# Kernel optimization log

Measured on AMD Instinct MI355X. Metric: run time of the kernel, lower is better.

The kernel has to match this reference:

```python
import jax, jax.numpy as jnp
import numpy as np

N_ITER = 4
NEG = -1e9


def _build_distmask(n):
    # dists='' -> 2 groups: upper triangular (j>i) and lower triangular (j<i); diag excluded
    iu = jnp.triu(jnp.ones((n, n), jnp.float32), 1)
    return jnp.stack([iu, iu.T], axis=0)  # (2, n, n)


def setup_inputs() -> dict:
    key = jax.random.key(0)
    k1, k2, k3 = jax.random.split(key, 3)
    B, N, D, H, G = 16, 256, 128, 8, 64
    x = jax.random.normal(k1, (B, N, D), jnp.float32)
    mask = jnp.ones((B, N), jnp.int32)
    ternary = jax.random.normal(k2, (2, D, D, H), jnp.float32)
    global_ = jax.random.normal(k3, (G, D, H), jnp.float32) / np.sqrt(D).astype(np.float32)
    return {"x": x, "mask": mask, "ternary": ternary, "global_": global_}


def reference(x, mask, ternary, global_):
    # x: (B,N,D) unary scores; mask: (B,N); ternary: (2,D,D,H); global_: (G,D,H)
    B, N, D = x.shape
    dm = _build_distmask(N)                       # (2,N,N)
    m1 = mask != 0                                # (B,N) valid tokens
    m2 = m1[:, :, None] & m1[:, None, :]          # (B,N,N) valid pairs
    pair_bias = jnp.where(m2[:, None, :, :], 0.0, NEG)  # (B,1,N,N); global cols stay unmasked

    Q_Z = x
    for _ in range(N_ITER):
        qz = jax.nn.softmax(Q_Z, axis=-1)         # (B,N,D) q(Z_i)
        # left[k,b,i,c,h] = sum_a qz[b,i,a] * ternary[k,a,c,h]
        left = jnp.einsum('bia,kach->kbich', qz, ternary)
        # H-node scores over local candidates: F[b,h,i,j] = sum_k dm[k,i,j] * sum_c left[k,b,i,c,h] qz[b,j,c]
        Fk = jnp.einsum('kbich,bjc->kbhij', left, qz)
        F = jnp.einsum('kbhij,kij->bhij', Fk, dm) + pair_bias
        # H-node scores over global candidates: G[b,h,i,g] = sum_a qz[b,i,a] global_[g,a,h]
        Gs = jnp.einsum('bia,gah->bhig', qz, global_)
        S = jnp.concatenate([F, Gs], axis=-1)     # (B,H,N,N+G), all-attn: joint softmax
        qh = jax.nn.softmax(S, axis=-1)           # async update: fresh q(H) used for Z update
        qh_loc, qh_glb = qh[..., :N], qh[..., N:]
        qhd = qh_loc[None] * dm[:, None, None]    # (2,B,H,N,N) distance-gated q(H)
        # right[k,b,j,a,h] = sum_c ternary[k,a,c,h] qz[b,j,c]  (message payload toward Z_i)
        right = jnp.einsum('kach,bjc->kbjah', ternary, qz)
        M1 = jnp.einsum('kbhij,kbjah->bia', qhd, right)   # message to dependent Z_i
        M2 = jnp.einsum('kbhij,kbich->bjc', qhd, left)    # message to head Z_j (block_msg=False)
        MG = jnp.einsum('bhig,gah->bia', qh_glb, global_)  # message from global nodes
        Q_Z = x + M1 + M2 + MG                    # regularize_Z=1, stepsize=1, damping=0
    return Q_Z                                    # output_prob=False -> unnormalized scores
```

## Files before the change

kernel.cpp:

```cpp
#include <hip/hip_runtime.h>
#include <hip/hip_bf16.h>

using bf16 = __hip_bfloat16;
typedef __bf16 bf16x8 __attribute__((ext_vector_type(8)));
typedef float f32x4 __attribute__((ext_vector_type(4)));
typedef unsigned short u16x8 __attribute__((ext_vector_type(8)));
typedef unsigned short u16x4 __attribute__((ext_vector_type(4)));

constexpr int B_ = 16, H_ = 8;
constexpr int BN = 4096;
constexpr int SW = 320;
constexpr float FNEG = -1000000000.0f;
constexpr size_t KOFF = (size_t)8 * 16 * 128 * 256;

__device__ __forceinline__ float b2f(bf16 v){ return __bfloat162float(v); }
__device__ __forceinline__ bf16 f2b(float v){ return __float2bfloat16(v); }
__device__ __forceinline__ bf16x8 ldf(const bf16* p){ return *(const bf16x8*)p; }
__device__ __forceinline__ f32x4 mfma16(bf16x8 a, bf16x8 b, f32x4 c){
  return __builtin_amdgcn_mfma_f32_16x16x32_bf16(a, b, c, 0, 0, 0);
}

__global__ __launch_bounds__(256) void k_prep(const float* __restrict__ tern,
                                              const float* __restrict__ glb,
                                              bf16* __restrict__ TL, bf16* __restrict__ TR,
                                              bf16* __restrict__ GB, bf16* __restrict__ GT){
  int t = blockIdx.x*256 + threadIdx.x;
  {
    int kh = t>>14, rest = t&16383;
    int k = kh>>3, h = kh&7;
    int r = rest>>7, cc = rest&127;
    TL[t] = f2b(tern[(((size_t)k*128 + cc)*128 + r)*8 + h]);
    TR[t] = f2b(tern[(((size_t)k*128 + r)*128 + cc)*8 + h]);
  }
  if (t < 65536){
    int h = t>>13, rest = t&8191;
    { int g = rest>>7, a = rest&127;
      GB[t] = f2b(glb[((size_t)g*128 + a)*8 + h]); }
    { int a = rest>>6, g = rest&63;
      GT[t] = f2b(glb[((size_t)g*128 + a)*8 + h]); }
  }
}

__global__ __launch_bounds__(256) void k_softmax_qz(const float* __restrict__ Q,
                                                    bf16* __restrict__ qzb){
  int row = blockIdx.x*4 + (threadIdx.x>>6);
  int lane = threadIdx.x&63;
  const float* q = Q + (size_t)row*128;
  float v0 = q[lane], v1 = q[lane+64];
  float m = fmaxf(v0, v1);
  #pragma unroll
  for (int o=32;o;o>>=1) m = fmaxf(m, __shfl_xor(m, o));
  float e0 = __expf(v0-m), e1 = __expf(v1-m), s = e0+e1;
  #pragma unroll
  for (int o=32;o;o>>=1) s += __shfl_xor(s, o);
  float inv = 1.f/s;
  bf16* o_ = qzb + (size_t)row*128;
  o_[lane] = f2b(e0*inv); o_[lane+64] = f2b(e1*inv);
}

__global__ __launch_bounds__(256) void k_proj(const bf16* __restrict__ qzb,
                                              const bf16* __restrict__ TL,
                                              const bf16* __restrict__ TR,
                                              bf16* __restrict__ left,
                                              bf16* __restrict__ LT2,
                                              bf16* __restrict__ RT2){
  const int z = blockIdx.z; const int kh = z & 15; const bool rightP = z >= 16;
  const int wi = threadIdx.x>>7, wj = (threadIdx.x>>6)&1;
  const int lane = threadIdx.x&63, lr = lane&15, kg = lane>>4;
  const int rb0 = blockIdx.x*64, cb = blockIdx.y*64;
  const int r0 = rb0 + wi*32, c0 = cb + wj*32;
  const bf16* A  = qzb + (size_t)r0*128;
  const bf16* Bb = (rightP ? TR : TL) + ((size_t)kh*128 + c0)*128;
  f32x4 acc[2][2] = {};
  #pragma unroll
  for (int k0=0;k0<128;k0+=32){
    bf16x8 a0 = ldf(A  + (size_t)lr*128      + k0 + kg*8);
    bf16x8 a1 = ldf(A  + (size_t)(lr+16)*128 + k0 + kg*8);
    bf16x8 b0 = ldf(Bb + (size_t)lr*128      + k0 + kg*8);
    bf16x8 b1 = ldf(Bb + (size_t)(lr+16)*128 + k0 + kg*8);
    acc[0][0]=mfma16(a0,b0,acc[0][0]); acc[0][1]=mfma16(a0,b1,acc[0][1]);
    acc[1][0]=mfma16(a1,b0,acc[1][0]); acc[1][1]=mfma16(a1,b1,acc[1][1]);
  }
  __shared__ unsigned short tl[64][68];
  #pragma unroll
  for (int fi=0;fi<2;fi++)
    #pragma unroll
    for (int fj=0;fj<2;fj++){
      u16x4 pk;
      #pragma unroll
      for (int r=0;r<4;r++) pk[r] = __builtin_bit_cast(unsigned short, f2b(acc[fi][fj][r]));
      *(u16x4*)&tl[wj*32 + fj*16 + lr][wi*32 + fi*16 + kg*4] = pk;
    }
  if (!rightP){
    #pragma unroll
    for (int fi=0;fi<2;fi++){
      int rb = r0 + fi*16 + kg*4;
      #pragma unroll
      for (int fj=0;fj<2;fj++){
        int col = c0 + fj*16 + lr;
        #pragma unroll
        for (int r=0;r<4;r++)
          left[((size_t)kh*BN + rb + r)*128 + col] = f2b(acc[fi][fj][r]);
      }
    }
  }
  __syncthreads();
  const int b = rb0 >> 8, jloc = rb0 & 255;
  const int col = threadIdx.x >> 2, seg = threadIdx.x & 3;
  bf16* O = rightP ? RT2 : LT2;
  unsigned short* dst = (unsigned short*)O +
      (((size_t)kh*16 + b)*128 + cb + col)*256 + jloc + seg*16;
  const unsigned short* src = &tl[col][seg*16];
  #pragma unroll
  for (int e=0;e<4;e++) *(u16x4*)(dst + e*4) = *(const u16x4*)(src + e*4);
}

__global__ __launch_bounds__(256) void k_FS(const bf16* __restrict__ qzb,
                                            const bf16* __restrict__ left,
                                            const bf16* __restrict__ GB,
                                            const int* __restrict__ mask,
                                            bf16* __restrict__ S){
  const int bh = blockIdx.z, b = bh>>3, h = bh&7;
  const int wi = threadIdx.x>>7, wj = (threadIdx.x>>6)&1;
  const int lane = threadIdx.x&63, lr = lane&15, kg = lane>>4;
  const int i0 = blockIdx.x*64 + wi*32;
  const bf16* qzB = qzb + (size_t)b*256*128;
  f32x4 acc[2][2] = {};
  if (blockIdx.y == 4){
    const bf16* A  = qzB + (size_t)i0*128;
    const bf16* Bb = GB + ((size_t)h*64 + wj*32)*128;
    #pragma unroll
    for (int k0=0;k0<128;k0+=32){
      bf16x8 a0=ldf(A +(size_t)lr*128+k0+kg*8), a1=ldf(A +(size_t)(lr+16)*128+k0+kg*8);
      bf16x8 b0=ldf(Bb+(size_t)lr*128+k0+kg*8), b1=ldf(Bb+(size_t)(lr+16)*128+k0+kg*8);
      acc[0][0]=mfma16(a0,b0,acc[0][0]); acc[0][1]=mfma16(a0,b1,acc[0][1]);
      acc[1][0]=mfma16(a1,b0,acc[1][0]); acc[1][1]=mfma16(a1,b1,acc[1][1]);
    }
    #pragma unroll
    for (int fi=0;fi<2;fi++)
      #pragma unroll
      for (int fj=0;fj<2;fj++)
        #pragma unroll
        for (int r=0;r<4;r++){
          int i = i0 + fi*16 + kg*4 + r, g = wj*32 + fj*16 + lr;
          S[((size_t)bh*256 + i)*SW + 256 + g] = f2b(acc[fi][fj][r]);
        }
    return;
  }
  const int j0 = blockIdx.y*64 + wj*32;
  const bool dual = (blockIdx.x == blockIdx.y);
  const bf16* Q  = qzB + (size_t)j0*128;
  const bf16* L0 = left + ((size_t)h*BN     + b*256 + i0)*128;
  const bf16* L1 = left + ((size_t)(8+h)*BN + b*256 + i0)*128;
  const bf16* Ls = (blockIdx.y > blockIdx.x) ? L0 : L1;
  f32x4 acc1[2][2] = {};
  #pragma unroll
  for (int k0=0;k0<128;k0+=32){
    bf16x8 b0=ldf(Q+(size_t)lr*128+k0+kg*8), b1=ldf(Q+(size_t)(lr+16)*128+k0+kg*8);
    if (!dual){
      bf16x8 a0=ldf(Ls+(size_t)lr*128+k0+kg*8), a1=ldf(Ls+(size_t)(lr+16)*128+k0+kg*8);
      acc[0][0]=mfma16(a0,b0,acc[0][0]); acc[0][1]=mfma16(a0,b1,acc[0][1]);
      acc[1][0]=mfma16(a1,b0,acc[1][0]); acc[1][1]=mfma16(a1,b1,acc[1][1]);
    } else {
      bf16x8 a0=ldf(L0+(size_t)lr*128+k0+kg*8), a1=ldf(L0+(size_t)(lr+16)*128+k0+kg*8);
      acc[0][0]=mfma16(a0,b0,acc[0][0]); acc[0][1]=mfma16(a0,b1,acc[0][1]);
      acc[1][0]=mfma16(a1,b0,acc[1][0]); acc[1][1]=mfma16(a1,b1,acc[1][1]);
      bf16x8 c0=ldf(L1+(size_t)lr*128+k0+kg*8), c1=ldf(L1+(size_t)(lr+16)*128+k0+kg*8);
      acc1[0][0]=mfma16(c0,b0,acc1[0][0]); acc1[0][1]=mfma16(c0,b1,acc1[0][1]);
      acc1[1][0]=mfma16(c1,b0,acc1[1][0]); acc1[1][1]=mfma16(c1,b1,acc1[1][1]);
    }
  }
  const int* mb = mask + b*256;
  #pragma unroll
  for (int fi=0;fi<2;fi++){
    #pragma unroll
    for (int r=0;r<4;r++){
      int i = i0 + fi*16 + kg*4 + r;
      int mi = mb[i];
      #pragma unroll
      for (int fj=0;fj<2;fj++){
        int j = j0 + fj*16 + lr;
        float v = acc[fi][fj][r];
        if (dual) v = (j>i) ? acc[fi][fj][r] : ((j<i) ? acc1[fi][fj][r] : 0.f);
        float bias = (mi && mb[j]) ? 0.f : FNEG;
        S[((size_t)bh*256 + i)*SW + j] = f2b(v + bias);
      }
    }
  }
}

__global__ __launch_bounds__(256) void k_softmax_T(const bf16* __restrict__ S,
                                                   bf16* __restrict__ qh,
                                                   bf16* __restrict__ qhT2){
  const int bh = blockIdx.y, i0 = blockIdx.x*64;
  __shared__ unsigned short t2[256][68];
  const int sub = threadIdx.x>>6, lane = threadIdx.x&63;
  for (int rr=0; rr<16; rr++){
    const int r = rr*4 + sub;
    const bf16* p = S + ((size_t)bh*256 + i0 + r)*SW;
    float v[5];
    #pragma unroll
    for (int e=0;e<5;e++) v[e] = b2f(p[lane + e*64]);
    float m = v[0];
    #pragma unroll
    for (int e=1;e<5;e++) m = fmaxf(m, v[e]);
    #pragma unroll
    for (int o=32;o;o>>=1) m = fmaxf(m, __shfl_xor(m, o));
    float s = 0.f;
    #pragma unroll
    for (int e=0;e<5;e++){ v[e] = __expf(v[e]-m); s += v[e]; }
    #pragma unroll
    for (int o=32;o;o>>=1) s += __shfl_xor(s, o);
    float inv = 1.f/s;
    bf16* o_ = qh + ((size_t)bh*256 + i0 + r)*SW;
    #pragma unroll
    for (int e=0;e<5;e++){
      bf16 ov = f2b(v[e]*inv);
      o_[lane + e*64] = ov;
      if (e < 4) t2[lane + e*64][r] = __builtin_bit_cast(unsigned short, ov);
    }
  }
  __syncthreads();
  const int j = threadIdx.x;
  unsigned short* dst = (unsigned short*)qhT2 + (((size_t)bh*4 + blockIdx.x)*256 + j)*64;
  #pragma unroll
  for (int e0=0;e0<64;e0+=4)
    *(u16x4*)(dst + e0) = *(const u16x4*)&t2[j][e0];
}

template<int MODE>
__global__ __launch_bounds__(256) void k_M(const bf16* __restrict__ Aall,
                                           const bf16* __restrict__ Bg_,
                                           const bf16* __restrict__ Bl_,
                                           const bf16* __restrict__ GT,
                                           float* __restrict__ Mp){
  const int z = blockIdx.z, b = z>>2, hg = z&3;
  const int wi = threadIdx.x>>7, wj = (threadIdx.x>>6)&1;
  const int lane = threadIdx.x&63, lr = lane&15, kg = lane>>4;
  const int r0 = blockIdx.x*64 + wi*32;
  const int c0 = blockIdx.y*64 + wj*32;
  f32x4 acc[2][2] = {};
  #pragma unroll
  for (int hh=0;hh<2;hh++){
    const int h = hg*2 + hh;
    const bf16* Bgh = Bg_ + (((size_t)h*16 + b)*128)*256;
    const bf16* Blh = Bl_ + (((size_t)h*16 + b)*128)*256;
    const bf16* A0 = (MODE==0) ? Aall + ((size_t)(b*8+h)*256)*SW
                               : Aall + ((size_t)(b*8+h)*4)*256*64;
    for (int kt=0;kt<8;kt++){
      const int k0 = kt*32;
      bf16x8 bg0 = ldf(Bgh + (size_t)(c0+lr)*256    + k0 + kg*8);
      bf16x8 bg1 = ldf(Bgh + (size_t)(c0+16+lr)*256 + k0 + kg*8);
      bf16x8 bl0 = ldf(Blh + (size_t)(c0+lr)*256    + k0 + kg*8);
      bf16x8 bl1 = ldf(Blh + (size_t)(c0+16+lr)*256 + k0 + kg*8);
      #pragma unroll
      for (int fi=0;fi<2;fi++){
        const int ib = r0 + fi*16;
        bf16x8 a;
        if constexpr (MODE==0)
          a = ldf(A0 + (size_t)(ib+lr)*SW + k0 + kg*8);
        else
          a = ldf(A0 + (((size_t)(k0>>6))*256 + ib + lr)*64 + (k0&63) + kg*8);
        if (k0 >= ib + 16){
          acc[fi][0]=mfma16(a,bg0,acc[fi][0]); acc[fi][1]=mfma16(a,bg1,acc[fi][1]);
        } else if (k0 + 32 <= ib){
          acc[fi][0]=mfma16(a,bl0,acc[fi][0]); acc[fi][1]=mfma16(a,bl1,acc[fi][1]);
        } else {
          u16x8 u = __builtin_bit_cast(u16x8, a), ug, ul;
          const int tt = k0 + kg*8 - ib - lr;
          #pragma unroll
          for (int e=0;e<8;e++){
            ug[e] = (tt+e>0) ? u[e] : (unsigned short)0;
            ul[e] = (tt+e<0) ? u[e] : (unsigned short)0;
          }
          bf16x8 ag = __builtin_bit_cast(bf16x8, ug), al = __builtin_bit_cast(bf16x8, ul);
          acc[fi][0]=mfma16(ag,bg0,acc[fi][0]); acc[fi][1]=mfma16(ag,bg1,acc[fi][1]);
          acc[fi][0]=mfma16(al,bl0,acc[fi][0]); acc[fi][1]=mfma16(al,bl1,acc[fi][1]);
        }
      }
    }
    if constexpr (MODE==0){
      const bf16* Bgl = GT + (size_t)h*128*64;
      #pragma unroll
      for (int kt=0;kt<2;kt++){
        const int k0 = kt*32;
        bf16x8 b0 = ldf(Bgl + (size_t)(c0+lr)*64    + k0 + kg*8);
        bf16x8 b1 = ldf(Bgl + (size_t)(c0+16+lr)*64 + k0 + kg*8);
        #pragma unroll
        for (int fi=0;fi<2;fi++){
          bf16x8 a = ldf(A0 + (size_t)(r0+fi*16+lr)*SW + 256 + k0 + kg*8);
          acc[fi][0]=mfma16(a,b0,acc[fi][0]); acc[fi][1]=mfma16(a,b1,acc[fi][1]);
        }
      }
    }
  }
  #pragma unroll
  for (int fi=0;fi<2;fi++)
    #pragma unroll
    for (int fj=0;fj<2;fj++)
      #pragma unroll
      for (int r=0;r<4;r++){
        int row = r0 + fi*16 + kg*4 + r;
        int col = c0 + fj*16 + lr;
        float* d = Mp + ((size_t)hg*BN + b*256 + row)*128 + col;
        if constexpr (MODE==1) *d += acc[fi][fj][r]; else *d = acc[fi][fj][r];
      }
}

__global__ __launch_bounds__(256) void k_redqz(const float* __restrict__ x,
                                               const float* __restrict__ Mp,
                                               float* __restrict__ out,
                                               bf16* __restrict__ qzb){
  const int row = blockIdx.x*4 + (threadIdx.x>>6);
  const int lane = threadIdx.x&63;
  const size_t base = (size_t)row*128;
  float v0 = x[base + lane], v1 = x[base + 64 + lane];
  #pragma unroll
  for (int g=0;g<4;g++){
    v0 += Mp[(size_t)g*524288 + base + lane];
    v1 += Mp[(size_t)g*524288 + base + 64 + lane];
  }
  out[base + lane] = v0; out[base + 64 + lane] = v1;
  float m = fmaxf(v0, v1);
  #pragma unroll
  for (int o=32;o;o>>=1) m = fmaxf(m, __shfl_xor(m, o));
  float e0 = __expf(v0-m), e1 = __expf(v1-m), s = e0+e1;
  #pragma unroll
  for (int o=32;o;o>>=1) s += __shfl_xor(s, o);
  float inv = 1.f/s;
  qzb[base + lane] = f2b(e0*inv); qzb[base + 64 + lane] = f2b(e1*inv);
}

extern "C" void kernel_launch(void* const* d_in, const int* in_sizes, int n_in,
                              void* d_out, int out_size, void* d_ws, size_t ws_size,
                              hipStream_t stream) {
  (void)in_sizes; (void)n_in; (void)out_size; (void)ws_size;
  const float* x    = (const float*)d_in[0];
  const int*   mask = (const int*)d_in[1];
  const float* tern = (const float*)d_in[2];
  const float* glb  = (const float*)d_in[3];
  float* out = (float*)d_out;

  char* w = (char*)d_ws;
  auto alloc = [&](size_t bytes){ void* p = (void*)w; w += (bytes + 255) & ~(size_t)255; return p; };
  bf16* qzb   = (bf16*) alloc((size_t)BN*128*2);
  bf16* left  = (bf16*) alloc((size_t)16*BN*128*2);
  bf16* LT2   = (bf16*) alloc((size_t)16*16*128*256*2);
  bf16* RT2   = (bf16*) alloc((size_t)16*16*128*256*2);
  bf16* S     = (bf16*) alloc((size_t)128*256*SW*2);
  bf16* qh    = (bf16*) alloc((size_t)128*256*SW*2);
  bf16* qhT2  = (bf16*) alloc((size_t)128*4*256*64*2);
  float* Mp   = (float*)alloc((size_t)4*BN*128*4);
  bf16* TL    = (bf16*) alloc((size_t)16*128*128*2);
  bf16* TR    = (bf16*) alloc((size_t)16*128*128*2);
  bf16* GB    = (bf16*) alloc((size_t)8*64*128*2);
  bf16* GT    = (bf16*) alloc((size_t)8*64*128*2);

  k_prep<<<1024, 256, 0, stream>>>(tern, glb, TL, TR, GB, GT);
  k_softmax_qz<<<1024, 256, 0, stream>>>(x, qzb);

  for (int it = 0; it < 4; ++it){
    k_proj<<<dim3(64,2,32), 256, 0, stream>>>(qzb, TL, TR, left, LT2, RT2);
    k_FS<<<dim3(4,5,128), 256, 0, stream>>>(qzb, left, GB, mask, S);
    k_softmax_T<<<dim3(4,128), 256, 0, stream>>>(S, qh, qhT2);
    k_M<0><<<dim3(4,2,64), 256, 0, stream>>>(qh, RT2, RT2 + KOFF, GT, Mp);
    k_M<1><<<dim3(4,2,64), 256, 0, stream>>>(qhT2, LT2 + KOFF, LT2, GT, Mp);
    k_redqz<<<1024, 256, 0, stream>>>(x, Mp, out, qzb);
  }
}
```

Before: 676.2 us.

## Fuse score GEMM with softmax and merge both message GEMMs into one launch

The score computation (local and global) is fused with the row softmax in one kernel that keeps a full 320-wide row slab in registers, then writes qh and its transpose through shared memory. This removes the intermediate S buffer round-trip and one launch. The two message kernels are merged into a single launch writing separate partial planes (8 instead of 4), so the read-modify-write accumulate is gone and k_redqz sums 8 planes. The merged kernel also skips loading B tiles that the triangular masking does not use. In exchange the fused kernel uses many more accumulator registers (20 f32x4) and launches far fewer blocks, which may hurt occupancy.

```diff
diff --git a/kernel.cpp b/kernel.cpp
--- a/kernel.cpp
+++ b/kernel.cpp
@@ -115,126 +115,118 @@
   for (int e=0;e<4;e++) *(u16x4*)(dst + e*4) = *(const u16x4*)(src + e*4);
 }
 
-__global__ __launch_bounds__(256) void k_FS(const bf16* __restrict__ qzb,
-                                            const bf16* __restrict__ left,
-                                            const bf16* __restrict__ GB,
-                                            const int* __restrict__ mask,
-                                            bf16* __restrict__ S){
-  const int bh = blockIdx.z, b = bh>>3, h = bh&7;
-  const int wi = threadIdx.x>>7, wj = (threadIdx.x>>6)&1;
-  const int lane = threadIdx.x&63, lr = lane&15, kg = lane>>4;
-  const int i0 = blockIdx.x*64 + wi*32;
+__global__ __launch_bounds__(256) void k_FSM(const bf16* __restrict__ qzb,
+                                             const bf16* __restrict__ left,
+                                             const bf16* __restrict__ GB,
+                                             const int* __restrict__ mask,
+                                             bf16* __restrict__ qh,
+                                             bf16* __restrict__ qhT2){
+  const int bh = blockIdx.y, b = bh>>3, h = bh&7;
+  const int ib4 = blockIdx.x;
+  const int w = threadIdx.x>>6, lane = threadIdx.x&63;
+  const int lr = lane&15, kg = lane>>4;
+  const int i0 = ib4*64, iw = i0 + w*16;
+  const int fd = iw>>4;
   const bf16* qzB = qzb + (size_t)b*256*128;
-  f32x4 acc[2][2] = {};
-  if (blockIdx.y == 4){
-    const bf16* A  = qzB + (size_t)i0*128;
-    const bf16* Bb = GB + ((size_t)h*64 + wj*32)*128;
-    #pragma unroll
-    for (int k0=0;k0<128;k0+=32){
-      bf16x8 a0=ldf(A +(size_t)lr*128+k0+kg*8), a1=ldf(A +(size_t)(lr+16)*128+k0+kg*8);
-      bf16x8 b0=ldf(Bb+(size_t)lr*128+k0+kg*8), b1=ldf(Bb+(size_t)(lr+16)*128+k0+kg*8);
-      acc[0][0]=mfma16(a0,b0,acc[0][0]); acc[0][1]=mfma16(a0,b1,acc[0][1]);
-      acc[1][0]=mfma16(a1,b0,acc[1][0]); acc[1][1]=mfma16(a1,b1,acc[1][1]);
-    }
-    #pragma unroll
-    for (int fi=0;fi<2;fi++)
-      #pragma unroll
-      for (int fj=0;fj<2;fj++)
-        #pragma unroll
-        for (int r=0;r<4;r++){
-          int i = i0 + fi*16 + kg*4 + r, g = wj*32 + fj*16 + lr;
-          S[((size_t)bh*256 + i)*SW + 256 + g] = f2b(acc[fi][fj][r]);
+  const bf16* L0 = left + ((size_t)h*BN     + b*256 + iw)*128;
+  const bf16* L1 = left + ((size_t)(8+h)*BN + b*256 + iw)*128;
+  const bf16* GBh = GB + (size_t)h*64*128;
+  f32x4 acc[20] = {}; f32x4 accD = {};
+  #pragma unroll
+  for (int k0=0;k0<128;k0+=32){
+    bf16x8 aQ  = ldf(qzB + (size_t)(iw+lr)*128 + k0 + kg*8);
+    bf16x8 aL0 = ldf(L0 + (size_t)lr*128 + k0 + kg*8);
+    bf16x8 aL1 = ldf(L1 + (size_t)lr*128 + k0 + kg*8);
+    #pragma unroll
+    for (int f=0;f<16;f++){
+      bf16x8 bf_ = ldf(qzB + (size_t)(f*16+lr)*128 + k0 + kg*8);
+      acc[f] = mfma16((f>=fd)? aL0 : aL1, bf_, acc[f]);
+      if (f==fd) accD = mfma16(aL1, bf_, accD);
+    }
+    #pragma unroll
+    for (int f2=0;f2<4;f2++){
+      bf16x8 bg = ldf(GBh + (size_t)(f2*16+lr)*128 + k0 + kg*8);
+      acc[16+f2] = mfma16(aQ, bg, acc[16+f2]);
+    }
+  }
+  const int* mb = mask + b*256;
+  int mi[4];
+  #pragma unroll
+  for (int r=0;r<4;r++) mi[r] = mb[iw + kg*4 + r];
+  float m[4] = {-3e38f,-3e38f,-3e38f,-3e38f};
+  #pragma unroll
+  for (int f=0;f<20;f++){
+    if (f<16){
+      int mj = mb[f*16 + lr];
+      #pragma unroll
+      for (int r=0;r<4;r++){
+        float v = acc[f][r];
+        if (f==fd){
+          int d = lr - (kg*4+r);
+          v = d>0 ? acc[f][r] : (d<0 ? accD[r] : 0.f);
         }
-    return;
-  }
-  const int j0 = blockIdx.y*64 + wj*32;
-  const bool dual = (blockIdx.x == blockIdx.y);
-  const bf16* Q  = qzB + (size_t)j0*128;
-  const bf16* L0 = left + ((size_t)h*BN     + b*256 + i0)*128;
-  const bf16* L1 = left + ((size_t)(8+h)*BN + b*256 + i0)*128;
-  const bf16* Ls = (blockIdx.y > blockIdx.x) ? L0 : L1;
-  f32x4 acc1[2][2] = {};
-  #pragma unroll
-  for (int k0=0;k0<128;k0+=32){
-    bf16x8 b0=ldf(Q+(size_t)lr*128+k0+kg*8), b1=ldf(Q+(size_t)(lr+16)*128+k0+kg*8);
-    if (!dual){
-      bf16x8 a0=ldf(Ls+(size_t)lr*128+k0+kg*8), a1=ldf(Ls+(size_t)(lr+16)*128+k0+kg*8);
-      acc[0][0]=mfma16(a0,b0,acc[0][0]); acc[0][1]=mfma16(a0,b1,acc[0][1]);
-      acc[1][0]=mfma16(a1,b0,acc[1][0]); acc[1][1]=mfma16(a1,b1,acc[1][1]);
+        v += (mi[r] && mj) ? 0.f : FNEG;
+        acc[f][r] = v;
+        m[r] = fmaxf(m[r], v);
+      }
     } else {
-      bf16x8 a0=ldf(L0+(size_t)lr*128+k0+kg*8), a1=ldf(L0+(size_t)(lr+16)*128+k0+kg*8);
-      acc[0][0]=mfma16(a0,b0,acc[0][0]); acc[0][1]=mfma16(a0,b1,acc[0][1]);
-      acc[1][0]=mfma16(a1,b0,acc[1][0]); acc[1][1]=mfma16(a1,b1,acc[1][1]);
-      bf16x8 c0=ldf(L1+(size_t)lr*128+k0+kg*8), c1=ldf(L1+(size_t)(lr+16)*128+k0+kg*8);
-      acc1[0][0]=mfma16(c0,b0,acc1[0][0]); acc1[0][1]=mfma16(c0,b1,acc1[0][1]);
-      acc1[1][0]=mfma16(c1,b0,acc1[1][0]); acc1[1][1]=mfma16(c1,b1,acc1[1][1]);
-    }
-  }
-  const int* mb = mask + b*256;
-  #pragma unroll
-  for (int fi=0;fi<2;fi++){
-    #pragma unroll
-    for (int r=0;r<4;r++){
-      int i = i0 + fi*16 + kg*4 + r;
-      int mi = mb[i];
-      #pragma unroll
-      for (int fj=0;fj<2;fj++){
-        int j = j0 + fj*16 + lr;
-        float v = acc[fi][fj][r];
-        if (dual) v = (j>i) ? acc[fi][fj][r] : ((j<i) ? acc1[fi][fj][r] : 0.f);
-        float bias = (mi && mb[j]) ? 0.f : FNEG;
-        S[((size_t)bh*256 + i)*SW + j] = f2b(v + bias);
-      }
-    }
-  }
-}
-
-__global__ __launch_bounds__(256) void k_softmax_T(const bf16* __restrict__ S,
-                                                   bf16* __restrict__ qh,
-                                                   bf16* __restrict__ qhT2){
-  const int bh = blockIdx.y, i0 = blockIdx.x*64;
-  __shared__ unsigned short t2[256][68];
-  const int sub = threadIdx.x>>6, lane = threadIdx.x&63;
-  for (int rr=0; rr<16; rr++){
-    const int r = rr*4 + sub;
-    const bf16* p = S + ((size_t)bh*256 + i0 + r)*SW;
-    float v[5];
-    #pragma unroll
-    for (int e=0;e<5;e++) v[e] = b2f(p[lane + e*64]);
-    float m = v[0];
-    #pragma unroll
-    for (int e=1;e<5;e++) m = fmaxf(m, v[e]);
-    #pragma unroll
-    for (int o=32;o;o>>=1) m = fmaxf(m, __shfl_xor(m, o));
-    float s = 0.f;
-    #pragma unroll
-    for (int e=0;e<5;e++){ v[e] = __expf(v[e]-m); s += v[e]; }
-    #pragma unroll
-    for (int o=32;o;o>>=1) s += __shfl_xor(s, o);
-    float inv = 1.f/s;
-    bf16* o_ = qh + ((size_t)bh*256 + i0 + r)*SW;
-    #pragma unroll
-    for (int e=0;e<5;e++){
-      bf16 ov = f2b(v[e]*inv);
-      o_[lane + e*64] = ov;
-      if (e < 4) t2[lane + e*64][r] = __builtin_bit_cast(unsigned short, ov);
-    }
+      #pragma unroll
+      for (int r=0;r<4;r++) m[r] = fmaxf(m[r], acc[f][r]);
+    }
+  }
+  #pragma unroll
+  for (int o=1;o<16;o<<=1)
+    #pragma unroll
+    for (int r=0;r<4;r++) m[r] = fmaxf(m[r], __shfl_xor(m[r], o));
+  float s[4] = {0.f,0.f,0.f,0.f};
+  #pragma unroll
+  for (int f=0;f<20;f++)
+    #pragma unroll
+    for (int r=0;r<4;r++){ float e = __expf(acc[f][r]-m[r]); acc[f][r]=e; s[r]+=e; }
+  #pragma unroll
+  for (int o=1;o<16;o<<=1)
+    #pragma unroll
+    for (int r=0;r<4;r++) s[r] += __shfl_xor(s[r], o);
+  float inv[4];
+  #pragma unroll
+  for (int r=0;r<4;r++) inv[r] = 1.f/s[r];
+  __shared__ unsigned short t2[320][72];
+  const int rowb = w*16 + kg*4;
+  #pragma unroll
+  for (int f=0;f<20;f++){
+    u16x4 pk;
+    #pragma unroll
+    for (int r=0;r<4;r++) pk[r] = __builtin_bit_cast(unsigned short, f2b(acc[f][r]*inv[r]));
+    *(u16x4*)&t2[f*16+lr][rowb] = pk;
   }
   __syncthreads();
-  const int j = threadIdx.x;
-  unsigned short* dst = (unsigned short*)qhT2 + (((size_t)bh*4 + blockIdx.x)*256 + j)*64;
-  #pragma unroll
-  for (int e0=0;e0<64;e0+=4)
-    *(u16x4*)(dst + e0) = *(const u16x4*)&t2[j][e0];
-}
-
-template<int MODE>
-__global__ __launch_bounds__(256) void k_M(const bf16* __restrict__ Aall,
-                                           const bf16* __restrict__ Bg_,
-                                           const bf16* __restrict__ Bl_,
-                                           const bf16* __restrict__ GT,
-                                           float* __restrict__ Mp){
-  const int z = blockIdx.z, b = z>>2, hg = z&3;
+  {
+    const int j = threadIdx.x;
+    unsigned short* dst = (unsigned short*)qhT2 + (((size_t)bh*4 + ib4)*256 + j)*64;
+    #pragma unroll
+    for (int e0=0;e0<64;e0+=8) *(u16x8*)(dst+e0) = *(const u16x8*)&t2[j][e0];
+  }
+  {
+    const int row = threadIdx.x&63, seg = threadIdx.x>>6;
+    unsigned short* dst = (unsigned short*)qh + ((size_t)bh*256 + i0 + row)*SW + seg*80;
+    #pragma unroll
+    for (int cc=0;cc<10;cc++){
+      u16x8 pk;
+      #pragma unroll
+      for (int e=0;e<8;e++) pk[e] = t2[seg*80 + cc*8 + e][row];
+      *(u16x8*)(dst + cc*8) = pk;
+    }
+  }
+}
+
+__global__ __launch_bounds__(256) void k_M2x(const bf16* __restrict__ qh,
+                                             const bf16* __restrict__ qhT2,
+                                             const bf16* __restrict__ RT2,
+                                             const bf16* __restrict__ LT2,
+                                             const bf16* __restrict__ GT,
+                                             float* __restrict__ Mp){
+  const int z = blockIdx.z;
+  const int mode = z>>6, zz = z&63, b = zz>>2, hg = zz&3;
   const int wi = threadIdx.x>>7, wj = (threadIdx.x>>6)&1;
   const int lane = threadIdx.x&63, lr = lane&15, kg = lane>>4;
   const int r0 = blockIdx.x*64 + wi*32;
@@ -243,24 +235,29 @@
   #pragma unroll
   for (int hh=0;hh<2;hh++){
     const int h = hg*2 + hh;
-    const bf16* Bgh = Bg_ + (((size_t)h*16 + b)*128)*256;
-    const bf16* Blh = Bl_ + (((size_t)h*16 + b)*128)*256;
-    const bf16* A0 = (MODE==0) ? Aall + ((size_t)(b*8+h)*256)*SW
-                               : Aall + ((size_t)(b*8+h)*4)*256*64;
+    const bf16* Bg = (mode ? LT2+KOFF : RT2) + ((size_t)h*16 + b)*128*256;
+    const bf16* Bl = (mode ? LT2 : RT2+KOFF) + ((size_t)h*16 + b)*128*256;
+    const bf16* A0 = mode ? qhT2 + (size_t)(b*8+h)*65536
+                          : qh   + (size_t)(b*8+h)*256*SW;
+    #pragma unroll
     for (int kt=0;kt<8;kt++){
       const int k0 = kt*32;
-      bf16x8 bg0 = ldf(Bgh + (size_t)(c0+lr)*256    + k0 + kg*8);
-      bf16x8 bg1 = ldf(Bgh + (size_t)(c0+16+lr)*256 + k0 + kg*8);
-      bf16x8 bl0 = ldf(Blh + (size_t)(c0+lr)*256    + k0 + kg*8);
-      bf16x8 bl1 = ldf(Blh + (size_t)(c0+16+lr)*256 + k0 + kg*8);
+      const bool needG = (k0 >= r0), needL = (k0 <= r0+32);
+      bf16x8 bg0{}, bg1{}, bl0{}, bl1{};
+      if (needG){
+        bg0 = ldf(Bg + (size_t)(c0+lr)*256    + k0 + kg*8);
+        bg1 = ldf(Bg + (size_t)(c0+16+lr)*256 + k0 + kg*8);
+      }
+      if (needL){
+        bl0 = ldf(Bl + (size_t)(c0+lr)*256    + k0 + kg*8);
+        bl1 = ldf(Bl + (size_t)(c0+16+lr)*256 + k0 + kg*8);
+      }
       #pragma unroll
       for (int fi=0;fi<2;fi++){
         const int ib = r0 + fi*16;
-        bf16x8 a;
-        if constexpr (MODE==0)
-          a = ldf(A0 + (size_t)(ib+lr)*SW + k0 + kg*8);
-        else
-          a = ldf(A0 + (((size_t)(k0>>6))*256 + ib + lr)*64 + (k0&63) + kg*8);
+        bf16x8 a = (mode==0)
+          ? ldf(A0 + (size_t)(ib+lr)*SW + k0 + kg*8)
+          : ldf(A0 + (((size_t)(k0>>6))*256 + ib + lr)*64 + (k0&63) + kg*8);
         if (k0 >= ib + 16){
           acc[fi][0]=mfma16(a,bg0,acc[fi][0]); acc[fi][1]=mfma16(a,bg1,acc[fi][1]);
         } else if (k0 + 32 <= ib){
@@ -279,7 +276,7 @@
         }
       }
     }
-    if constexpr (MODE==0){
+    if (mode==0){
       const bf16* Bgl = GT + (size_t)h*128*64;
       #pragma unroll
       for (int kt=0;kt<2;kt++){
@@ -294,6 +291,7 @@
       }
     }
   }
+  const int plane = mode*4 + hg;
   #pragma unroll
   for (int fi=0;fi<2;fi++)
     #pragma unroll
@@ -302,8 +300,7 @@
       for (int r=0;r<4;r++){
         int row = r0 + fi*16 + kg*4 + r;
         int col = c0 + fj*16 + lr;
-        float* d = Mp + ((size_t)hg*BN + b*256 + row)*128 + col;
-        if constexpr (MODE==1) *d += acc[fi][fj][r]; else *d = acc[fi][fj][r];
+        Mp[((size_t)plane*BN + b*256 + row)*128 + col] = acc[fi][fj][r];
       }
 }
 
@@ -316,7 +313,7 @@
   const size_t base = (size_t)row*128;
   float v0 = x[base + lane], v1 = x[base + 64 + lane];
   #pragma unroll
-  for (int g=0;g<4;g++){
+  for (int g=0;g<8;g++){
     v0 += Mp[(size_t)g*524288 + base + lane];
     v1 += Mp[(size_t)g*524288 + base + 64 + lane];
   }
@@ -347,10 +344,9 @@
   bf16* left  = (bf16*) alloc((size_t)16*BN*128*2);
   bf16* LT2   = (bf16*) alloc((size_t)16*16*128*256*2);
   bf16* RT2   = (bf16*) alloc((size_t)16*16*128*256*2);
-  bf16* S     = (bf16*) alloc((size_t)128*256*SW*2);
   bf16* qh    = (bf16*) alloc((size_t)128*256*SW*2);
   bf16* qhT2  = (bf16*) alloc((size_t)128*4*256*64*2);
-  float* Mp   = (float*)alloc((size_t)4*BN*128*4);
+  float* Mp   = (float*)alloc((size_t)8*BN*128*4);
   bf16* TL    = (bf16*) alloc((size_t)16*128*128*2);
   bf16* TR    = (bf16*) alloc((size_t)16*128*128*2);
   bf16* GB    = (bf16*) alloc((size_t)8*64*128*2);
@@ -361,10 +357,8 @@
 
   for (int it = 0; it < 4; ++it){
     k_proj<<<dim3(64,2,32), 256, 0, stream>>>(qzb, TL, TR, left, LT2, RT2);
-    k_FS<<<dim3(4,5,128), 256, 0, stream>>>(qzb, left, GB, mask, S);
-    k_softmax_T<<<dim3(4,128), 256, 0, stream>>>(S, qh, qhT2);
-    k_M<0><<<dim3(4,2,64), 256, 0, stream>>>(qh, RT2, RT2 + KOFF, GT, Mp);
-    k_M<1><<<dim3(4,2,64), 256, 0, stream>>>(qhT2, LT2 + KOFF, LT2, GT, Mp);
+    k_FSM<<<dim3(4,128), 256, 0, stream>>>(qzb, left, GB, mask, qh, qhT2);
+    k_M2x<<<dim3(4,2,128), 256, 0, stream>>>(qh, qhT2, RT2, LT2, GT, Mp);
     k_redqz<<<1024, 256, 0, stream>>>(x, Mp, out, qzb);
   }
 }
```

After: 551.0 us. -18.5%, faster.
